# Optimization experiments

Measured on AMD Instinct MI355X. Metric: run time of the kernel, lower is better.

Reference implementation:

```python
import jax, jax.numpy as jnp
import numpy as np

EPS = 1e-20
STRIDE, PADDING, DILATION = 1, 2, 1


def setup_inputs() -> dict:
    key = jax.random.key(0)
    ks = jax.random.split(key, 8)
    B, C, O, H, W, K = 8, 32, 32, 256, 256, 5
    return {
        "d": jax.random.uniform(ks[0], (B, C, H, W), jnp.float32) + 0.1,   # positive depth
        "cd": jax.random.uniform(ks[1], (B, C, H, W), jnp.float32),        # depth confidence in [0,1)
        "gx": jax.random.normal(ks[2], (B, C, H, W), jnp.float32),         # x-gradient
        "cgx": jax.random.uniform(ks[3], (B, C, H, W), jnp.float32),       # gradient confidence
        "w_prop": jax.random.normal(ks[4], (1, C, 1, 1), jnp.float32) * 0.1,
        "spatial_weight": jax.random.normal(ks[5], (C, 1, K, K), jnp.float32) * 0.1,
        "channel_weight": jax.random.normal(ks[6], (O, C, 1, 1), jnp.float32) * 0.1,
        "bias": jax.random.normal(ks[7], (1, O, 1, 1), jnp.float32) * 0.01,
    }


def _conv(x, w, groups, stride=1, padding=0, dilation=1):
    return jax.lax.conv_general_dilated(
        x, w, (stride, stride), ((padding, padding), (padding, padding)),
        rhs_dilation=(dilation, dilation),
        dimension_numbers=("NCHW", "OIHW", "NCHW"),
        feature_group_count=groups)


def reference(d, cd, gx, cgx, w_prop, spatial_weight, channel_weight, bias):
    in_channels = d.shape[1]
    # EnforcePos reparameterization: effective weights = softplus(raw)
    wp = jax.nn.softplus(w_prop)
    sw = jax.nn.softplus(spatial_weight)
    cw = jax.nn.softplus(channel_weight)

    pad_w = lambda x, lr: jnp.pad(x, ((0, 0), (0, 0), (0, 0), lr))
    d_left = pad_w(d[..., :-1], (0, 1))
    cd_left = pad_w(cd[..., :-1], (0, 1))
    d_right = pad_w(d[..., 1:], (1, 0))
    cd_right = pad_w(cd[..., 1:], (1, 0))

    cgx_from_ds = cd_left * cd_right
    height = (cd_left * d_left + cd_right * d_right) / (cd_left + cd_right + EPS)
    gx_from_ds = (d_right - d_left) / 2 / (height + EPS)

    gx_prop = (wp * cgx * gx + cgx_from_ds * gx_from_ds) / (wp * cgx + cgx_from_ds + EPS)
    cgx_prop = (wp * cgx + cgx_from_ds) / (wp + 1)

    # depthwise spatial conv (groups = in_channels), then 1x1 channel conv
    nom = _conv(cgx_prop * gx_prop, sw, in_channels, STRIDE, PADDING, DILATION)
    denom = _conv(cgx_prop, sw, in_channels, STRIDE, PADDING, DILATION)
    gx_s = nom / (denom + EPS)
    cgx_s = denom / jnp.sum(sw)

    nom = _conv(cgx_s * gx_s, cw, 1)
    denom = _conv(cgx_s, cw, 1)
    gx_out = nom / (denom + EPS) + bias
    cgx_out = denom / jnp.sum(cw)
    return (gx_out * STRIDE, cgx_out / (STRIDE * STRIDE))
```

## Files before the change

### kernel.cpp

```cpp
#include <hip/hip_runtime.h>
#include <math.h>

constexpr int IMG_H = 256;
constexpr int IMG_W = 256;
constexpr int NB = 8;
constexpr int NC = 32;
constexpr int NO = 32;
constexpr int PLANE = IMG_H * IMG_W;
constexpr int HALF = NB * NC * PLANE;

constexpr int ATH = 64;
constexpr int ATW = 64;
constexpr int ARH = ATH + 4;
constexpr int ARW = ATW + 4;
constexpr int AREG = ARH * ARW;

#define EPSV 1e-20f

__device__ __forceinline__ float rcpf_(float x) { return __builtin_amdgcn_rcpf(x); }
__device__ __forceinline__ float softplusf_(float x) {
  return fmaxf(x, 0.0f) + log1pf(expf(-fabsf(x)));
}

__global__ void weights_kernel(const float* __restrict__ wp_raw,
                               const float* __restrict__ sw_raw,
                               const float* __restrict__ cw_raw,
                               float* __restrict__ ws) {
  __shared__ float red[256];
  const int t = threadIdx.x;
  if (t < 32) ws[t] = softplusf_(wp_raw[t]);
  float ssum = 0.f;
  for (int i = t; i < NC * 25; i += 256) {
    float v = softplusf_(sw_raw[i]);
    ws[32 + i] = v;
    ssum += v;
  }
  float csum = 0.f;
  for (int i = t; i < NO * NC; i += 256) {
    float v = softplusf_(cw_raw[i]);
    int o = i >> 5, c = i & 31;
    ws[832 + c * NO + o] = v;
    csum += v;
  }
  red[t] = ssum; __syncthreads();
  for (int off = 128; off; off >>= 1) { if (t < off) red[t] += red[t + off]; __syncthreads(); }
  const float S_sw = red[0];
  __syncthreads();
  red[t] = csum; __syncthreads();
  for (int off = 128; off; off >>= 1) { if (t < off) red[t] += red[t + off]; __syncthreads(); }
  if (t == 0) { ws[1856] = S_sw; ws[1857] = red[0]; }
}

__device__ __forceinline__ void pointwise_pv(
    float dv, float cdv, float gxv, float cgv, int gw,
    float wpc, float inv_wp1, float& Pv, float& Vv) {
  float dl  = (gw == IMG_W - 1) ? 0.f : dv;
  float cdl = (gw == IMG_W - 1) ? 0.f : cdv;
  float dr  = (gw == 0) ? 0.f : dv;
  float cdr = (gw == 0) ? 0.f : cdv;
  float cfd = cdl * cdr;
  float height = (cdl * dl + cdr * dr) * rcpf_(cdl + cdr + EPSV);
  float gfd = (dr - dl) * 0.5f * rcpf_(height + EPSV);
  float den = fmaf(wpc, cgv, cfd);
  float num = fmaf(wpc * cgv, gxv, cfd * gfd);
  float gprop = num * rcpf_(den + EPSV);
  float cprop = den * inv_wp1;
  Pv = cprop;
  Vv = cprop * gprop;
}

__global__ __launch_bounds__(256, 4) void kernelA(
    const float* __restrict__ dp, const float* __restrict__ cdp,
    const float* __restrict__ gxp, const float* __restrict__ cgxp,
    const float* __restrict__ ws, float* __restrict__ out) {
  __shared__ __align__(16) float Pbuf[AREG];
  __shared__ __align__(16) float Vbuf[AREG];

  const int t = threadIdx.x;
  const int tile = blockIdx.x;
  const int c = blockIdx.y;
  const int b = blockIdx.z;
  const int h0 = (tile >> 2) * ATH;
  const int w0t = (tile & 3) * ATW;

  const float wpc = ws[c];
  const float inv_wp1 = rcpf_(wpc + 1.0f);
  const float inv_Ssw = rcpf_(ws[1856]);
  const int plane = (b * NC + c) * PLANE;

  #pragma unroll 1
  for (int chunk = 0; chunk < 2; ++chunk) {
    float rd[9], rc[9], rg[9], rcg[9], rm[9];
    int rgw[9];
    #pragma unroll
    for (int k = 0; k < 9; ++k) {
      int i = t + (chunk * 9 + k) * 256;
      int rr = i / ARW;
      int col = i - rr * ARW;
      int gh = h0 + rr - 2;
      int gw = w0t + col - 2;
      bool inb = ((unsigned)gh < (unsigned)IMG_H) & ((unsigned)gw < (unsigned)IMG_W);
      int ghc = min(max(gh, 0), IMG_H - 1);
      int gwc = min(max(gw, 0), IMG_W - 1);
      int idx = plane + ghc * IMG_W + gwc;
      rd[k] = dp[idx];
      rc[k] = cdp[idx];
      rg[k] = gxp[idx];
      rcg[k] = cgxp[idx];
      rm[k] = inb ? 1.0f : 0.0f;
      rgw[k] = gw;
    }
    #pragma unroll
    for (int k = 0; k < 9; ++k) {
      int i = t + (chunk * 9 + k) * 256;
      float Pv, Vv;
      pointwise_pv(rd[k], rc[k] * rm[k], rg[k], rcg[k] * rm[k], rgw[k],
                   wpc, inv_wp1, Pv, Vv);
      Pbuf[i] = Pv;
      Vbuf[i] = Vv;
    }
  }
  if (t < 16) {
    int i = t + 18 * 256;
    int rr = i / ARW;
    int col = i - rr * ARW;
    int gh = h0 + rr - 2;
    int gw = w0t + col - 2;
    bool inb = ((unsigned)gh < (unsigned)IMG_H) & ((unsigned)gw < (unsigned)IMG_W);
    int ghc = min(max(gh, 0), IMG_H - 1);
    int gwc = min(max(gw, 0), IMG_W - 1);
    int idx = plane + ghc * IMG_W + gwc;
    float m = inb ? 1.0f : 0.0f;
    float Pv, Vv;
    pointwise_pv(dp[idx], cdp[idx] * m, gxp[idx], cgxp[idx] * m, gw,
                 wpc, inv_wp1, Pv, Vv);
    Pbuf[i] = Pv;
    Vbuf[i] = Vv;
  }

  float sww[25];
  #pragma unroll
  for (int k2 = 0; k2 < 25; ++k2) sww[k2] = ws[32 + c * 25 + k2];

  __syncthreads();

  #pragma unroll
  for (int j = 0; j < 2; ++j) {
    int tau = t + j * 256;
    int row = tau >> 3;
    int w0l = (tau & 7) * 8;
    float den8[8], nom8[8];
    #pragma unroll
    for (int q = 0; q < 8; ++q) { den8[q] = 0.f; nom8[q] = 0.f; }
    #pragma unroll
    for (int kr = 0; kr < 5; ++kr) {
      int base = (row + kr) * ARW + w0l;
      const float4* p4 = (const float4*)&Pbuf[base];
      const float4* v4 = (const float4*)&Vbuf[base];
      float4 pa = p4[0], pb = p4[1], pc = p4[2];
      float4 va = v4[0], vb = v4[1], vc = v4[2];
      float pr[12] = {pa.x, pa.y, pa.z, pa.w, pb.x, pb.y, pb.z, pb.w,
                      pc.x, pc.y, pc.z, pc.w};
      float vr[12] = {va.x, va.y, va.z, va.w, vb.x, vb.y, vb.z, vb.w,
                      vc.x, vc.y, vc.z, vc.w};
      #pragma unroll
      for (int kc = 0; kc < 5; ++kc) {
        float wv = sww[kr * 5 + kc];
        #pragma unroll
        for (int q = 0; q < 8; ++q) {
          den8[q] = fmaf(wv, pr[kc + q], den8[q]);
          nom8[q] = fmaf(wv, vr[kc + q], nom8[q]);
        }
      }
    }
    float s0[8], u0[8];
    #pragma unroll
    for (int q = 0; q < 8; ++q) {
      float dw = den8[q];
      float s = dw * inv_Ssw;
      float gxs = nom8[q] * rcpf_(dw + EPSV);
      s0[q] = s;
      u0[q] = s * gxs;
    }
    int gidx = plane + (h0 + row) * IMG_W + w0t + w0l;
    float4* sg = (float4*)&out[gidx];
    float4* ug = (float4*)&out[HALF + gidx];
    sg[0] = make_float4(s0[0], s0[1], s0[2], s0[3]);
    sg[1] = make_float4(s0[4], s0[5], s0[6], s0[7]);
    ug[0] = make_float4(u0[0], u0[1], u0[2], u0[3]);
    ug[1] = make_float4(u0[4], u0[5], u0[6], u0[7]);
  }
}

__global__ __launch_bounds__(256, 4) void kernelB(
    float* __restrict__ out, const float* __restrict__ ws,
    const float* __restrict__ bias) {
  __shared__ __align__(16) float wlds[NC * NO];
  __shared__ float blds[NO];

  const int t = threadIdx.x;
  ((float4*)wlds)[t] = ((const float4*)(ws + 832))[t];
  if (t < NO) blds[t] = bias[t];
  const float inv_Scw = rcpf_(ws[1857]);
  __syncthreads();

  const int og = __builtin_amdgcn_readfirstlane(t >> 6);
  const int lane = t & 63;
  const int b = blockIdx.y;
  const int hw = blockIdx.x * 256 + lane * 4;
  const int idx0 = b * NC * PLANE + hw;

  float4 accn[8], accd[8];
  #pragma unroll
  for (int o = 0; o < 8; ++o) {
    accn[o] = make_float4(0.f, 0.f, 0.f, 0.f);
    accd[o] = make_float4(0.f, 0.f, 0.f, 0.f);
  }

  #pragma unroll 8
  for (int c = 0; c < NC; ++c) {
    const float4 s4 = *(const float4*)&out[idx0 + c * PLANE];
    const float4 u4 = *(const float4*)&out[HALF + idx0 + c * PLANE];
    const float* w8 = &wlds[c * NO + og * 8];
    #pragma unroll
    for (int o = 0; o < 8; ++o) {
      float wv = w8[o];
      accn[o].x = fmaf(wv, u4.x, accn[o].x);
      accn[o].y = fmaf(wv, u4.y, accn[o].y);
      accn[o].z = fmaf(wv, u4.z, accn[o].z);
      accn[o].w = fmaf(wv, u4.w, accn[o].w);
      accd[o].x = fmaf(wv, s4.x, accd[o].x);
      accd[o].y = fmaf(wv, s4.y, accd[o].y);
      accd[o].z = fmaf(wv, s4.z, accd[o].z);
      accd[o].w = fmaf(wv, s4.w, accd[o].w);
    }
  }

  __syncthreads();

  #pragma unroll
  for (int o = 0; o < 8; ++o) {
    int oo = og * 8 + o;
    float bv = blds[oo];
    float4 dn = accd[o];
    float4 g, cg;
    g.x = fmaf(accn[o].x, rcpf_(dn.x + EPSV), bv);
    g.y = fmaf(accn[o].y, rcpf_(dn.y + EPSV), bv);
    g.z = fmaf(accn[o].z, rcpf_(dn.z + EPSV), bv);
    g.w = fmaf(accn[o].w, rcpf_(dn.w + EPSV), bv);
    cg.x = dn.x * inv_Scw; cg.y = dn.y * inv_Scw;
    cg.z = dn.z * inv_Scw; cg.w = dn.w * inv_Scw;
    int oidx = (b * NO + oo) * PLANE + hw;
    *(float4*)&out[oidx] = g;
    *(float4*)&out[HALF + oidx] = cg;
  }
}

extern "C" void kernel_launch(void* const* d_in, const int* in_sizes, int n_in,
                              void* d_out, int out_size, void* d_ws, size_t ws_size,
                              hipStream_t stream) {
  const float* dp   = (const float*)d_in[0];
  const float* cdp  = (const float*)d_in[1];
  const float* gxp  = (const float*)d_in[2];
  const float* cgxp = (const float*)d_in[3];
  const float* wp   = (const float*)d_in[4];
  const float* sw   = (const float*)d_in[5];
  const float* cw   = (const float*)d_in[6];
  const float* bias = (const float*)d_in[7];
  float* out = (float*)d_out;
  float* ws  = (float*)d_ws;

  weights_kernel<<<1, 256, 0, stream>>>(wp, sw, cw, ws);
  kernelA<<<dim3(16, NC, NB), 256, 0, stream>>>(dp, cdp, gxp, cgxp, ws, out);
  kernelB<<<dim3(PLANE / 256, NB), 256, 0, stream>>>(out, ws, bias);
}
```

Baseline: 417.4 us.

## Vectorize halo staging, swizzle LDS tile, fold spatial normalization into channel stage

Kernel A now loads the haloed input tile as float4 quads, five loads per thread in an interleaved schedule, and stores P/V into a padded LDS tile whose column offsets are XOR-swizzled per row to reduce bank conflicts. The per-pixel spatial normalization (divide by the weight sum and by the denominator) is removed from kernel A. Kernel A now writes the raw den and nom sums, and kernel B folds the scale factors into a single constant and a rescaled epsilon. The aim is to cut global load instructions, LDS conflicts and ALU work, at the cost of more complex indexing. The algebraic folding changes epsilon semantics slightly. nom/den no longer equals the original gx_s*cgx_s product exactly, because the reference computes cgx_s*gx_s = den/S * nom/(den+eps), which is about nom/S.

```diff
diff --git a/kernel.cpp b/kernel.cpp
--- a/kernel.cpp
+++ b/kernel.cpp
@@ -11,11 +11,18 @@
 
 constexpr int ATH = 64;
 constexpr int ATW = 64;
-constexpr int ARH = ATH + 4;
-constexpr int ARW = ATW + 4;
-constexpr int AREG = ARH * ARW;
+constexpr int ARH2 = 68;
+constexpr int ARW2 = 72;
+constexpr int AROWB = ARW2 * 4;
+constexpr int VOFF = ARH2 * AROWB;
+constexpr int NQUAD = 18;
+constexpr int TOTQ = NQUAD * ARH2;
+static_assert(TOTQ == 1224, "quad task count");
 
 #define EPSV 1e-20f
+
+typedef float f4 __attribute__((ext_vector_type(4)));
+typedef float f2 __attribute__((ext_vector_type(2)));
 
 __device__ __forceinline__ float rcpf_(float x) { return __builtin_amdgcn_rcpf(x); }
 __device__ __forceinline__ float softplusf_(float x) {
@@ -73,8 +80,8 @@
     const float* __restrict__ dp, const float* __restrict__ cdp,
     const float* __restrict__ gxp, const float* __restrict__ cgxp,
     const float* __restrict__ ws, float* __restrict__ out) {
-  __shared__ __align__(16) float Pbuf[AREG];
-  __shared__ __align__(16) float Vbuf[AREG];
+  __shared__ __align__(16) float PVS[2 * ARH2 * ARW2];
+  char* shb = (char*)PVS;
 
   const int t = threadIdx.x;
   const int tile = blockIdx.x;
@@ -85,58 +92,66 @@
 
   const float wpc = ws[c];
   const float inv_wp1 = rcpf_(wpc + 1.0f);
-  const float inv_Ssw = rcpf_(ws[1856]);
   const int plane = (b * NC + c) * PLANE;
 
-  #pragma unroll 1
-  for (int chunk = 0; chunk < 2; ++chunk) {
-    float rd[9], rc[9], rg[9], rcg[9], rm[9];
-    int rgw[9];
-    #pragma unroll
-    for (int k = 0; k < 9; ++k) {
-      int i = t + (chunk * 9 + k) * 256;
-      int rr = i / ARW;
-      int col = i - rr * ARW;
-      int gh = h0 + rr - 2;
-      int gw = w0t + col - 2;
-      bool inb = ((unsigned)gh < (unsigned)IMG_H) & ((unsigned)gw < (unsigned)IMG_W);
-      int ghc = min(max(gh, 0), IMG_H - 1);
-      int gwc = min(max(gw, 0), IMG_W - 1);
-      int idx = plane + ghc * IMG_W + gwc;
-      rd[k] = dp[idx];
-      rc[k] = cdp[idx];
-      rg[k] = gxp[idx];
-      rcg[k] = cgxp[idx];
-      rm[k] = inb ? 1.0f : 0.0f;
-      rgw[k] = gw;
-    }
-    #pragma unroll
-    for (int k = 0; k < 9; ++k) {
-      int i = t + (chunk * 9 + k) * 256;
-      float Pv, Vv;
-      pointwise_pv(rd[k], rc[k] * rm[k], rg[k], rcg[k] * rm[k], rgw[k],
-                   wpc, inv_wp1, Pv, Vv);
-      Pbuf[i] = Pv;
-      Vbuf[i] = Vv;
-    }
-  }
-  if (t < 16) {
-    int i = t + 18 * 256;
-    int rr = i / ARW;
-    int col = i - rr * ARW;
-    int gh = h0 + rr - 2;
-    int gw = w0t + col - 2;
-    bool inb = ((unsigned)gh < (unsigned)IMG_H) & ((unsigned)gw < (unsigned)IMG_W);
-    int ghc = min(max(gh, 0), IMG_H - 1);
-    int gwc = min(max(gw, 0), IMG_W - 1);
-    int idx = plane + ghc * IMG_W + gwc;
-    float m = inb ? 1.0f : 0.0f;
-    float Pv, Vv;
-    pointwise_pv(dp[idx], cdp[idx] * m, gxp[idx], cgxp[idx] * m, gw,
-                 wpc, inv_wp1, Pv, Vv);
-    Pbuf[i] = Pv;
-    Vbuf[i] = Vv;
-  }
+#define STG_LOAD(r) \
+  const int i4_##r = t + 256 * (r); \
+  const int R_##r = i4_##r / NQUAD; \
+  const int jq_##r = i4_##r - NQUAD * R_##r; \
+  const int gh_##r = h0 + R_##r - 2; \
+  const int ghc_##r = min(max(gh_##r, 0), IMG_H - 1); \
+  const int g0_##r = w0t + 4 * jq_##r - 4; \
+  const int g0c_##r = min(max(g0_##r, 0), IMG_W - 4); \
+  const int gb_##r = plane + ghc_##r * IMG_W + g0c_##r; \
+  const f4 d4_##r = *(const f4*)(dp + gb_##r); \
+  const f4 c4_##r = *(const f4*)(cdp + gb_##r); \
+  const f4 g4_##r = *(const f4*)(gxp + gb_##r); \
+  const f4 x4_##r = *(const f4*)(cgxp + gb_##r);
+
+#define STG_PROC(r) \
+  { \
+    const bool act = (i4_##r < TOTQ); \
+    const bool rowv = ((unsigned)gh_##r < (unsigned)IMG_H); \
+    float Pq[4], Vq[4]; \
+    _Pragma("unroll") \
+    for (int q = 0; q < 4; ++q) { \
+      const int gw = g0_##r + q; \
+      const float m = (rowv & ((unsigned)gw < (unsigned)IMG_W)) ? 1.0f : 0.0f; \
+      pointwise_pv(d4_##r[q], c4_##r[q] * m, g4_##r[q], x4_##r[q] * m, gw, \
+                   wpc, inv_wp1, Pq[q], Vq[q]); \
+    } \
+    const int Rb = R_##r * AROWB; \
+    const unsigned pm = ((unsigned)(R_##r & 7)) << 4; \
+    const int x1 = 16 * jq_##r - 8; \
+    const int x2 = 16 * jq_##r; \
+    const int o1 = Rb + (int)((unsigned)x1 ^ (x1 < 256 ? pm : 0u)); \
+    const int o2 = Rb + (int)((unsigned)x2 ^ (x2 < 256 ? pm : 0u)); \
+    if (act & (jq_##r >= 1)) { \
+      f2 wp_; wp_[0] = Pq[0]; wp_[1] = Pq[1]; \
+      f2 wv_; wv_[0] = Vq[0]; wv_[1] = Vq[1]; \
+      *(f2*)(shb + o1) = wp_; \
+      *(f2*)(shb + VOFF + o1) = wv_; \
+    } \
+    if (act & (jq_##r <= 16)) { \
+      f2 wp_; wp_[0] = Pq[2]; wp_[1] = Pq[3]; \
+      f2 wv_; wv_[0] = Vq[2]; wv_[1] = Vq[3]; \
+      *(f2*)(shb + o2) = wp_; \
+      *(f2*)(shb + VOFF + o2) = wv_; \
+    } \
+  }
+
+  STG_LOAD(0)
+  STG_LOAD(1)
+  STG_LOAD(2)
+  STG_PROC(0)
+  STG_LOAD(3)
+  STG_PROC(1)
+  STG_LOAD(4)
+  STG_PROC(2)
+  STG_PROC(3)
+  STG_PROC(4)
+#undef STG_LOAD
+#undef STG_PROC
 
   float sww[25];
   #pragma unroll
@@ -145,24 +160,33 @@
   __syncthreads();
 
   #pragma unroll
-  for (int j = 0; j < 2; ++j) {
-    int tau = t + j * 256;
-    int row = tau >> 3;
-    int w0l = (tau & 7) * 8;
+  for (int jj = 0; jj < 2; ++jj) {
+    const int tau = t + jj * 256;
+    const int row = tau >> 3;
+    const int c7 = tau & 7;
+    const int X0 = 32 * c7;
+    const unsigned keep2 = (c7 == 7) ? 0u : 0x70u;
     float den8[8], nom8[8];
     #pragma unroll
     for (int q = 0; q < 8; ++q) { den8[q] = 0.f; nom8[q] = 0.f; }
     #pragma unroll
     for (int kr = 0; kr < 5; ++kr) {
-      int base = (row + kr) * ARW + w0l;
-      const float4* p4 = (const float4*)&Pbuf[base];
-      const float4* v4 = (const float4*)&Vbuf[base];
-      float4 pa = p4[0], pb = p4[1], pc = p4[2];
-      float4 va = v4[0], vb = v4[1], vc = v4[2];
-      float pr[12] = {pa.x, pa.y, pa.z, pa.w, pb.x, pb.y, pb.z, pb.w,
-                      pc.x, pc.y, pc.z, pc.w};
-      float vr[12] = {va.x, va.y, va.z, va.w, vb.x, vb.y, vb.z, vb.w,
-                      vc.x, vc.y, vc.z, vc.w};
+      const int R = row + kr;
+      const int Rb = R * AROWB;
+      const unsigned pm = ((unsigned)(R & 7)) << 4;
+      const int o0 = Rb + (int)((unsigned)X0 ^ pm);
+      const int o1 = Rb + (int)((unsigned)(X0 + 16) ^ pm);
+      const int o2 = Rb + (int)((unsigned)(X0 + 32) ^ (pm & keep2));
+      const f4 pa = *(const f4*)(shb + o0);
+      const f4 pb = *(const f4*)(shb + o1);
+      const f4 pc = *(const f4*)(shb + o2);
+      const f4 va = *(const f4*)(shb + VOFF + o0);
+      const f4 vb = *(const f4*)(shb + VOFF + o1);
+      const f4 vc = *(const f4*)(shb + VOFF + o2);
+      float pr[12] = {pa[0], pa[1], pa[2], pa[3], pb[0], pb[1], pb[2], pb[3],
+                      pc[0], pc[1], pc[2], pc[3]};
+      float vr[12] = {va[0], va[1], va[2], va[3], vb[0], vb[1], vb[2], vb[3],
+                      vc[0], vc[1], vc[2], vc[3]};
       #pragma unroll
       for (int kc = 0; kc < 5; ++kc) {
         float wv = sww[kr * 5 + kc];
@@ -173,22 +197,13 @@
         }
       }
     }
-    float s0[8], u0[8];
-    #pragma unroll
-    for (int q = 0; q < 8; ++q) {
-      float dw = den8[q];
-      float s = dw * inv_Ssw;
-      float gxs = nom8[q] * rcpf_(dw + EPSV);
-      s0[q] = s;
-      u0[q] = s * gxs;
-    }
-    int gidx = plane + (h0 + row) * IMG_W + w0t + w0l;
+    const int gidx = plane + (h0 + row) * IMG_W + w0t + 8 * c7;
     float4* sg = (float4*)&out[gidx];
     float4* ug = (float4*)&out[HALF + gidx];
-    sg[0] = make_float4(s0[0], s0[1], s0[2], s0[3]);
-    sg[1] = make_float4(s0[4], s0[5], s0[6], s0[7]);
-    ug[0] = make_float4(u0[0], u0[1], u0[2], u0[3]);
-    ug[1] = make_float4(u0[4], u0[5], u0[6], u0[7]);
+    sg[0] = make_float4(den8[0], den8[1], den8[2], den8[3]);
+    sg[1] = make_float4(den8[4], den8[5], den8[6], den8[7]);
+    ug[0] = make_float4(nom8[0], nom8[1], nom8[2], nom8[3]);
+    ug[1] = make_float4(nom8[4], nom8[5], nom8[6], nom8[7]);
   }
 }
 
@@ -201,7 +216,10 @@
   const int t = threadIdx.x;
   ((float4*)wlds)[t] = ((const float4*)(ws + 832))[t];
   if (t < NO) blds[t] = bias[t];
-  const float inv_Scw = rcpf_(ws[1857]);
+  const float Ssw = ws[1856];
+  const float Scw = ws[1857];
+  const float epsS = EPSV * Ssw;
+  const float scale = rcpf_(Ssw) * rcpf_(Scw);
   __syncthreads();
 
   const int og = __builtin_amdgcn_readfirstlane(t >> 6);
@@ -244,12 +262,12 @@
     float bv = blds[oo];
     float4 dn = accd[o];
     float4 g, cg;
-    g.x = fmaf(accn[o].x, rcpf_(dn.x + EPSV), bv);
-    g.y = fmaf(accn[o].y, rcpf_(dn.y + EPSV), bv);
-    g.z = fmaf(accn[o].z, rcpf_(dn.z + EPSV), bv);
-    g.w = fmaf(accn[o].w, rcpf_(dn.w + EPSV), bv);
-    cg.x = dn.x * inv_Scw; cg.y = dn.y * inv_Scw;
-    cg.z = dn.z * inv_Scw; cg.w = dn.w * inv_Scw;
+    g.x = fmaf(accn[o].x, rcpf_(dn.x + epsS), bv);
+    g.y = fmaf(accn[o].y, rcpf_(dn.y + epsS), bv);
+    g.z = fmaf(accn[o].z, rcpf_(dn.z + epsS), bv);
+    g.w = fmaf(accn[o].w, rcpf_(dn.w + epsS), bv);
+    cg.x = dn.x * scale; cg.y = dn.y * scale;
+    cg.z = dn.z * scale; cg.w = dn.w * scale;
     int oidx = (b * NO + oo) * PLANE + hw;
     *(float4*)&out[oidx] = g;
     *(float4*)&out[HALF + oidx] = cg;
```

Result: no change. 417.1 us (-0.1%).

## Fuse depthwise and pointwise convs into one channel-looping tiled kernel

Applied to the files above, without the earlier changes.

Replaces the two-kernel pipeline, which wrote s/u intermediates to global memory and reread them, with one fused kernel. Each 512-thread block owns a 16x32 spatial tile, loops over all 32 input channels with double-buffered LDS halos and prefetches the next channel, then accumulates the 32 output channels in registers. The intent is to remove the intermediate global round trip. The cost is much more register pressure (64 accumulators), per-channel barriers, and fewer, larger blocks, which may reduce occupancy. The algebra is also simplified so the depthwise nom/denom ratio cancels, and a swizzled block-to-batch mapping is added.

```diff
diff --git a/kernel.cpp b/kernel.cpp
--- a/kernel.cpp
+++ b/kernel.cpp
@@ -9,13 +9,21 @@
 constexpr int PLANE = IMG_H * IMG_W;
 constexpr int HALF = NB * NC * PLANE;
 
-constexpr int ATH = 64;
-constexpr int ATW = 64;
-constexpr int ARH = ATH + 4;
-constexpr int ARW = ATW + 4;
-constexpr int AREG = ARH * ARW;
+constexpr int TW = 16;
+constexpr int TH = 32;
+constexpr int NT = TW * TH;
+constexpr int RR = TH + 4;
+constexpr int RCF = 24;
+constexpr int RSB = RCF * 4;
+constexpr int PXB = RR * RSB;
+constexpr int BUFB = 2 * PXB;
+constexpr int NTASK = RR * 12;
+constexpr int TILES = (IMG_W / TW) * (IMG_H / TH);
 
 #define EPSV 1e-20f
+
+typedef float f4 __attribute__((ext_vector_type(4)));
+typedef float f2 __attribute__((ext_vector_type(2)));
 
 __device__ __forceinline__ float rcpf_(float x) { return __builtin_amdgcn_rcpf(x); }
 __device__ __forceinline__ float softplusf_(float x) {
@@ -69,190 +77,117 @@
   Vv = cprop * gprop;
 }
 
-__global__ __launch_bounds__(256, 4) void kernelA(
+__global__ __launch_bounds__(NT, 4) void fused_kernel(
     const float* __restrict__ dp, const float* __restrict__ cdp,
     const float* __restrict__ gxp, const float* __restrict__ cgxp,
-    const float* __restrict__ ws, float* __restrict__ out) {
-  __shared__ __align__(16) float Pbuf[AREG];
-  __shared__ __align__(16) float Vbuf[AREG];
+    const float* __restrict__ ws, const float* __restrict__ bias,
+    float* __restrict__ out) {
+  __shared__ __align__(16) char shb[2 * BUFB];
 
   const int t = threadIdx.x;
-  const int tile = blockIdx.x;
-  const int c = blockIdx.y;
-  const int b = blockIdx.z;
-  const int h0 = (tile >> 2) * ATH;
-  const int w0t = (tile & 3) * ATW;
-
-  const float wpc = ws[c];
-  const float inv_wp1 = rcpf_(wpc + 1.0f);
-  const float inv_Ssw = rcpf_(ws[1856]);
-  const int plane = (b * NC + c) * PLANE;
+
+  const int wg = blockIdx.x + blockIdx.y * gridDim.x;
+  const int virt = (wg & 7) * TILES + (wg >> 3);
+  const int b = virt >> 7;
+  const int tile = virt & (TILES - 1);
+  const int tx = tile & 15, ty = tile >> 4;
+  const int w0 = tx * TW, h0 = ty * TH;
+
+  const float Ssw = ws[1856], Scw = ws[1857];
+  const float epsS = EPSV * Ssw;
+  const float oscale = rcpf_(Ssw) * rcpf_(Scw);
+
+  const bool tact = t < NTASK;
+  const int R = min(t, NTASK - 1) / 12;
+  const int hq = min(t, NTASK - 1) - R * 12;
+  const int gh = h0 + R - 2;
+  const int ghc = min(max(gh, 0), IMG_H - 1);
+  const int g0 = w0 - 4 + 2 * hq;
+  const int g0c = min(max(g0, 0), IMG_W - 2);
+  const int goff = ghc * IMG_W + g0c;
+  const bool rowv = (unsigned)gh < (unsigned)IMG_H;
+  const float m0 = (rowv & ((unsigned)g0 < (unsigned)IMG_W)) ? 1.f : 0.f;
+  const float m1 = (rowv & ((unsigned)(g0 + 1) < (unsigned)IMG_W)) ? 1.f : 0.f;
+  const int wb = R * RSB + hq * 8;
+
+  const int x = t & (TW - 1);
+  const int r = t >> 4;
+  const int cvb = r * RSB + (x + 2) * 4;
+  const int pixoff = (h0 + r) * IMG_W + (w0 + x);
+
+  const int planebase = b * NC * PLANE;
+
+  float accN[32], accD[32];
+  #pragma unroll
+  for (int o = 0; o < 32; ++o) { accN[o] = 0.f; accD[o] = 0.f; }
+
+  f2 vd, vc, vg, vx;
+  if (tact) {
+    vd = *(const f2*)(dp + planebase + goff);
+    vc = *(const f2*)(cdp + planebase + goff);
+    vg = *(const f2*)(gxp + planebase + goff);
+    vx = *(const f2*)(cgxp + planebase + goff);
+  }
 
   #pragma unroll 1
-  for (int chunk = 0; chunk < 2; ++chunk) {
-    float rd[9], rc[9], rg[9], rcg[9], rm[9];
-    int rgw[9];
-    #pragma unroll
-    for (int k = 0; k < 9; ++k) {
-      int i = t + (chunk * 9 + k) * 256;
-      int rr = i / ARW;
-      int col = i - rr * ARW;
-      int gh = h0 + rr - 2;
-      int gw = w0t + col - 2;
-      bool inb = ((unsigned)gh < (unsigned)IMG_H) & ((unsigned)gw < (unsigned)IMG_W);
-      int ghc = min(max(gh, 0), IMG_H - 1);
-      int gwc = min(max(gw, 0), IMG_W - 1);
-      int idx = plane + ghc * IMG_W + gwc;
-      rd[k] = dp[idx];
-      rc[k] = cdp[idx];
-      rg[k] = gxp[idx];
-      rcg[k] = cgxp[idx];
-      rm[k] = inb ? 1.0f : 0.0f;
-      rgw[k] = gw;
-    }
-    #pragma unroll
-    for (int k = 0; k < 9; ++k) {
-      int i = t + (chunk * 9 + k) * 256;
-      float Pv, Vv;
-      pointwise_pv(rd[k], rc[k] * rm[k], rg[k], rcg[k] * rm[k], rgw[k],
-                   wpc, inv_wp1, Pv, Vv);
-      Pbuf[i] = Pv;
-      Vbuf[i] = Vv;
-    }
-  }
-  if (t < 16) {
-    int i = t + 18 * 256;
-    int rr = i / ARW;
-    int col = i - rr * ARW;
-    int gh = h0 + rr - 2;
-    int gw = w0t + col - 2;
-    bool inb = ((unsigned)gh < (unsigned)IMG_H) & ((unsigned)gw < (unsigned)IMG_W);
-    int ghc = min(max(gh, 0), IMG_H - 1);
-    int gwc = min(max(gw, 0), IMG_W - 1);
-    int idx = plane + ghc * IMG_W + gwc;
-    float m = inb ? 1.0f : 0.0f;
-    float Pv, Vv;
-    pointwise_pv(dp[idx], cdp[idx] * m, gxp[idx], cgxp[idx] * m, gw,
-                 wpc, inv_wp1, Pv, Vv);
-    Pbuf[i] = Pv;
-    Vbuf[i] = Vv;
-  }
-
-  float sww[25];
-  #pragma unroll
-  for (int k2 = 0; k2 < 25; ++k2) sww[k2] = ws[32 + c * 25 + k2];
-
-  __syncthreads();
-
-  #pragma unroll
-  for (int j = 0; j < 2; ++j) {
-    int tau = t + j * 256;
-    int row = tau >> 3;
-    int w0l = (tau & 7) * 8;
-    float den8[8], nom8[8];
-    #pragma unroll
-    for (int q = 0; q < 8; ++q) { den8[q] = 0.f; nom8[q] = 0.f; }
+  for (int c = 0; c < NC; ++c) {
+    const int bsel = (c & 1) * BUFB;
+    const float wpc = ws[c];
+    const float inv_wp1 = rcpf_(wpc + 1.0f);
+
+    if (tact) {
+      float P0, V0, P1, V1;
+      pointwise_pv(vd[0], vc[0] * m0, vg[0], vx[0] * m0, g0,
+                   wpc, inv_wp1, P0, V0);
+      pointwise_pv(vd[1], vc[1] * m1, vg[1], vx[1] * m1, g0 + 1,
+                   wpc, inv_wp1, P1, V1);
+      f2 Pw; Pw[0] = P0; Pw[1] = P1;
+      f2 Vw; Vw[0] = V0; Vw[1] = V1;
+      *(f2*)(shb + bsel + wb) = Pw;
+      *(f2*)(shb + bsel + PXB + wb) = Vw;
+    }
+
+    if ((c + 1 < NC) & tact) {
+      const int pb = planebase + (c + 1) * PLANE + goff;
+      vd = *(const f2*)(dp + pb);
+      vc = *(const f2*)(cdp + pb);
+      vg = *(const f2*)(gxp + pb);
+      vx = *(const f2*)(cgxp + pb);
+    }
+
+    __syncthreads();
+
+    const char* bp = shb + bsel + cvb;
+    const float* swc = ws + 32 + c * 25;
+    float Dc = 0.f, Nc = 0.f;
     #pragma unroll
     for (int kr = 0; kr < 5; ++kr) {
-      int base = (row + kr) * ARW + w0l;
-      const float4* p4 = (const float4*)&Pbuf[base];
-      const float4* v4 = (const float4*)&Vbuf[base];
-      float4 pa = p4[0], pb = p4[1], pc = p4[2];
-      float4 va = v4[0], vb = v4[1], vc = v4[2];
-      float pr[12] = {pa.x, pa.y, pa.z, pa.w, pb.x, pb.y, pb.z, pb.w,
-                      pc.x, pc.y, pc.z, pc.w};
-      float vr[12] = {va.x, va.y, va.z, va.w, vb.x, vb.y, vb.z, vb.w,
-                      vc.x, vc.y, vc.z, vc.w};
       #pragma unroll
       for (int kc = 0; kc < 5; ++kc) {
-        float wv = sww[kr * 5 + kc];
-        #pragma unroll
-        for (int q = 0; q < 8; ++q) {
-          den8[q] = fmaf(wv, pr[kc + q], den8[q]);
-          nom8[q] = fmaf(wv, vr[kc + q], nom8[q]);
-        }
+        const float wv = swc[kr * 5 + kc];
+        const float pv = *(const float*)(bp + kr * RSB + kc * 4);
+        const float vv = *(const float*)(bp + PXB + kr * RSB + kc * 4);
+        Dc = fmaf(wv, pv, Dc);
+        Nc = fmaf(wv, vv, Nc);
       }
     }
-    float s0[8], u0[8];
+
+    const float* cwc = ws + 832 + c * NO;
     #pragma unroll
-    for (int q = 0; q < 8; ++q) {
-      float dw = den8[q];
-      float s = dw * inv_Ssw;
-      float gxs = nom8[q] * rcpf_(dw + EPSV);
-      s0[q] = s;
-      u0[q] = s * gxs;
-    }
-    int gidx = plane + (h0 + row) * IMG_W + w0t + w0l;
-    float4* sg = (float4*)&out[gidx];
-    float4* ug = (float4*)&out[HALF + gidx];
-    sg[0] = make_float4(s0[0], s0[1], s0[2], s0[3]);
-    sg[1] = make_float4(s0[4], s0[5], s0[6], s0[7]);
-    ug[0] = make_float4(u0[0], u0[1], u0[2], u0[3]);
-    ug[1] = make_float4(u0[4], u0[5], u0[6], u0[7]);
-  }
-}
-
-__global__ __launch_bounds__(256, 4) void kernelB(
-    float* __restrict__ out, const float* __restrict__ ws,
-    const float* __restrict__ bias) {
-  __shared__ __align__(16) float wlds[NC * NO];
-  __shared__ float blds[NO];
-
-  const int t = threadIdx.x;
-  ((float4*)wlds)[t] = ((const float4*)(ws + 832))[t];
-  if (t < NO) blds[t] = bias[t];
-  const float inv_Scw = rcpf_(ws[1857]);
-  __syncthreads();
-
-  const int og = __builtin_amdgcn_readfirstlane(t >> 6);
-  const int lane = t & 63;
-  const int b = blockIdx.y;
-  const int hw = blockIdx.x * 256 + lane * 4;
-  const int idx0 = b * NC * PLANE + hw;
-
-  float4 accn[8], accd[8];
+    for (int o = 0; o < 32; ++o) {
+      const float wv = cwc[o];
+      accD[o] = fmaf(wv, Dc, accD[o]);
+      accN[o] = fmaf(wv, Nc, accN[o]);
+    }
+  }
+
+  const int ob = b * NO * PLANE + pixoff;
   #pragma unroll
-  for (int o = 0; o < 8; ++o) {
-    accn[o] = make_float4(0.f, 0.f, 0.f, 0.f);
-    accd[o] = make_float4(0.f, 0.f, 0.f, 0.f);
-  }
-
-  #pragma unroll 8
-  for (int c = 0; c < NC; ++c) {
-    const float4 s4 = *(const float4*)&out[idx0 + c * PLANE];
-    const float4 u4 = *(const float4*)&out[HALF + idx0 + c * PLANE];
-    const float* w8 = &wlds[c * NO + og * 8];
-    #pragma unroll
-    for (int o = 0; o < 8; ++o) {
-      float wv = w8[o];
-      accn[o].x = fmaf(wv, u4.x, accn[o].x);
-      accn[o].y = fmaf(wv, u4.y, accn[o].y);
-      accn[o].z = fmaf(wv, u4.z, accn[o].z);
-      accn[o].w = fmaf(wv, u4.w, accn[o].w);
-      accd[o].x = fmaf(wv, s4.x, accd[o].x);
-      accd[o].y = fmaf(wv, s4.y, accd[o].y);
-      accd[o].z = fmaf(wv, s4.z, accd[o].z);
-      accd[o].w = fmaf(wv, s4.w, accd[o].w);
-    }
-  }
-
-  __syncthreads();
-
-  #pragma unroll
-  for (int o = 0; o < 8; ++o) {
-    int oo = og * 8 + o;
-    float bv = blds[oo];
-    float4 dn = accd[o];
-    float4 g, cg;
-    g.x = fmaf(accn[o].x, rcpf_(dn.x + EPSV), bv);
-    g.y = fmaf(accn[o].y, rcpf_(dn.y + EPSV), bv);
-    g.z = fmaf(accn[o].z, rcpf_(dn.z + EPSV), bv);
-    g.w = fmaf(accn[o].w, rcpf_(dn.w + EPSV), bv);
-    cg.x = dn.x * inv_Scw; cg.y = dn.y * inv_Scw;
-    cg.z = dn.z * inv_Scw; cg.w = dn.w * inv_Scw;
-    int oidx = (b * NO + oo) * PLANE + hw;
-    *(float4*)&out[oidx] = g;
-    *(float4*)&out[HALF + oidx] = cg;
+  for (int o = 0; o < 32; ++o) {
+    const float g = fmaf(accN[o], rcpf_(accD[o] + epsS), bias[o]);
+    const float cg = accD[o] * oscale;
+    out[ob + o * PLANE] = g;
+    out[HALF + ob + o * PLANE] = cg;
   }
 }
 
@@ -271,6 +206,6 @@
   float* ws  = (float*)d_ws;
 
   weights_kernel<<<1, 256, 0, stream>>>(wp, sw, cw, ws);
-  kernelA<<<dim3(16, NC, NB), 256, 0, stream>>>(dp, cdp, gxp, cgxp, ws, out);
-  kernelB<<<dim3(PLANE / 256, NB), 256, 0, stream>>>(out, ws, bias);
-}
+  fused_kernel<<<dim3(TILES, NB), NT, 0, stream>>>(dp, cdp, gxp, cgxp, ws,
+                                                   bias, out);
+}
```

Result: faster. 390.0 us (-6.6%).
